# Kernel optimization log

Measured on AMD Instinct MI355X. Metric: run time of the kernel, lower is better.

Reference implementation:

```python
import jax, jax.numpy as jnp
import numpy as np

N_NODES = 100000
N_EDGES = 1600000
NODE_DIM = 64
HIDDEN = 64
T = 11


def _init_linear(key, d_in, d_out, bias=True):
    kw, kb = jax.random.split(key)
    lim = 1.0 / np.sqrt(d_in)
    W = jax.random.uniform(kw, (d_in, d_out), jnp.float32, -lim, lim)
    if bias:
        b = jax.random.uniform(kb, (d_out,), jnp.float32, -lim, lim)
        return W, b
    return W


def setup_inputs() -> dict:
    key = jax.random.key(0)
    ks = jax.random.split(key, 10)
    x = jax.random.normal(ks[0], (N_NODES, NODE_DIM), jnp.float32)
    edge_index = jax.random.randint(ks[1], (2, N_EDGES), 0, N_NODES, jnp.int64)
    time_span = jnp.arange(T, dtype=jnp.float32)
    # SAGEConv params: W_neigh (lin_l, with bias) applied to mean-aggregated
    # neighbors, W_root (lin_r, no bias) applied to the node itself.
    W1n, b1 = _init_linear(ks[2], NODE_DIM, HIDDEN)
    W1r = _init_linear(ks[3], NODE_DIM, HIDDEN, bias=False)
    W2n, b2 = _init_linear(ks[4], HIDDEN, HIDDEN)
    W2r = _init_linear(ks[5], HIDDEN, HIDDEN, bias=False)
    W3n, b3 = _init_linear(ks[6], HIDDEN, NODE_DIM)
    W3r = _init_linear(ks[7], HIDDEN, NODE_DIM, bias=False)
    Wd, bd = _init_linear(ks[8], NODE_DIM, 2)
    return {
        "x": x, "edge_index": edge_index, "time_span": time_span,
        "W1n": W1n, "b1": b1, "W1r": W1r,
        "W2n": W2n, "b2": b2, "W2r": W2r,
        "W3n": W3n, "b3": b3, "W3r": W3r,
        "Wd": Wd, "bd": bd,
    }


def _sage_conv(x, src, dst, deg_inv, Wn, bn, Wr):
    # gather source features, mean-aggregate onto targets (PyG SAGEConv 'mean')
    agg = jax.ops.segment_sum(x[src], dst, num_segments=N_NODES)  # [N, d]
    mean = agg * deg_inv  # zero for isolated nodes
    return mean @ Wn + bn + x @ Wr


def reference(x, edge_index, time_span, W1n, b1, W1r, W2n, b2, W2r,
              W3n, b3, W3r, Wd, bd):
    src, dst = edge_index[0], edge_index[1]
    deg = jax.ops.segment_sum(jnp.ones((N_EDGES,), jnp.float32), dst,
                              num_segments=N_NODES)
    deg_inv = jnp.where(deg > 0, 1.0 / jnp.maximum(deg, 1.0), 0.0)[:, None]

    def ode_func(h):
        h1 = jax.nn.relu(_sage_conv(h, src, dst, deg_inv, W1n, b1, W1r))
        h2 = jax.nn.relu(_sage_conv(h1, src, dst, deg_inv, W2n, b2, W2r))
        return _sage_conv(h2, src, dst, deg_inv, W3n, b3, W3r)

    dts = time_span[1:] - time_span[:-1]  # euler fixed-step per interval

    def step(h, dt):
        h_new = h + dt * ode_func(h)
        return h_new, h_new

    _, xs = jax.lax.scan(step, x, dts)
    solution = jnp.concatenate([x[None], xs], axis=0)  # [T, N, node_dim]
    trajectories = solution @ Wd + bd  # [T, N, 2]
    return trajectories, solution
```

## Files before the change

### kernel.cpp

```cpp
#include <hip/hip_runtime.h>

#define NN 100000
#define NE 1600000
#define DIM 64
#define TT 11
#define NB_SCAN 391

typedef unsigned short u16;
typedef unsigned int u32;
typedef __attribute__((ext_vector_type(8))) short bf16x8;
typedef __attribute__((ext_vector_type(4))) float f32x4;

__device__ __forceinline__ u32 pack_bf16(float a, float b) {
    u32 ua = __float_as_uint(a);
    ua += 0x7fff + ((ua >> 16) & 1);
    u32 ub = __float_as_uint(b);
    ub += 0x7fff + ((ub >> 16) & 1);
    return (ua >> 16) | (ub & 0xffff0000u);
}

__global__ void k_deg(const int* __restrict__ dst, int* __restrict__ deg) {
    int e = blockIdx.x * blockDim.x + threadIdx.x;
    if (e < NE) atomicAdd(&deg[dst[e]], 1);
}

__global__ __launch_bounds__(256) void k_bsum(const int* __restrict__ deg,
                                              int* __restrict__ bsum) {
    __shared__ int s[256];
    int t = threadIdx.x;
    int i = blockIdx.x * 256 + t;
    s[t] = (i < NN) ? deg[i] : 0;
    __syncthreads();
    for (int off = 128; off >= 1; off >>= 1) {
        if (t < off) s[t] += s[t + off];
        __syncthreads();
    }
    if (t == 0) bsum[blockIdx.x] = s[0];
}

__global__ __launch_bounds__(512) void k_scan1(const int* __restrict__ bsum,
                                               int* __restrict__ bpre) {
    __shared__ int s[512];
    int t = threadIdx.x;
    int v0 = (t < NB_SCAN) ? bsum[t] : 0;
    s[t] = v0;
    __syncthreads();
    for (int off = 1; off < 512; off <<= 1) {
        int v = (t >= off) ? s[t - off] : 0;
        __syncthreads();
        s[t] += v;
        __syncthreads();
    }
    if (t < NB_SCAN) bpre[t] = s[t] - v0;
}

__global__ __launch_bounds__(256) void k_rowptr(const int* __restrict__ deg,
        const int* __restrict__ bpre, int* __restrict__ row_ptr,
        int* __restrict__ cursor, float* __restrict__ deg_inv) {
    __shared__ int s[256];
    int t = threadIdx.x;
    int i = blockIdx.x * 256 + t;
    int d = (i < NN) ? deg[i] : 0;
    s[t] = d;
    __syncthreads();
    for (int off = 1; off < 256; off <<= 1) {
        int v = (t >= off) ? s[t - off] : 0;
        __syncthreads();
        s[t] += v;
        __syncthreads();
    }
    if (i < NN) {
        int excl = bpre[blockIdx.x] + s[t] - d;
        row_ptr[i] = excl;
        cursor[i] = excl;
        deg_inv[i] = d > 0 ? 1.0f / (float)d : 0.0f;
        if (i == NN - 1) row_ptr[NN] = excl + d;
    }
}

__global__ void k_fill(const int* __restrict__ src, const int* __restrict__ dst,
        int* __restrict__ cursor, int* __restrict__ csr_src) {
    int e = blockIdx.x * blockDim.x + threadIdx.x;
    if (e < NE) {
        int p = atomicAdd(&cursor[dst[e]], 1);
        csr_src[p] = src[e];
    }
}

__global__ __launch_bounds__(256) void k_wprep(
        const float* __restrict__ W1n, const float* __restrict__ W1r,
        const float* __restrict__ W2n, const float* __restrict__ W2r,
        const float* __restrict__ W3n, const float* __restrict__ W3r,
        u16* __restrict__ Wt) {
    const float* Ws[6] = {W1n, W1r, W2n, W2r, W3n, W3r};
    const float* W = Ws[blockIdx.x];
    u16* o = Wt + blockIdx.x * 4096;
    int t = threadIdx.x;
    int n = t >> 2, kg = (t & 3) * 16;
    u32 pk[8];
#pragma unroll
    for (int j = 0; j < 8; ++j)
        pk[j] = pack_bf16(W[(kg + 2 * j) * 64 + n], W[(kg + 2 * j + 1) * 64 + n]);
    *(uint4*)(o + n * 64 + kg)     = make_uint4(pk[0], pk[1], pk[2], pk[3]);
    *(uint4*)(o + n * 64 + kg + 8) = make_uint4(pk[4], pk[5], pk[6], pk[7]);
}

__global__ __launch_bounds__(256) void k_gather(const u16* __restrict__ hb,
        const int* __restrict__ row_ptr, const int* __restrict__ csr_src,
        const float* __restrict__ deg_inv, u16* __restrict__ Mb) {
    int wid = (int)((blockIdx.x * blockDim.x + threadIdx.x) >> 6);
    int lane = threadIdx.x & 63;
    if (wid >= NN) return;
    int sub = lane >> 3;
    int d4 = lane & 7;
    int b = row_ptr[wid], e = row_ptr[wid + 1];
    float di = deg_inv[wid];
    float a0[8] = {0, 0, 0, 0, 0, 0, 0, 0};
    float a1[8] = {0, 0, 0, 0, 0, 0, 0, 0};
    int i = b;
    for (; i + 16 <= e; i += 16) {
        int n0 = csr_src[i + sub];
        int n1 = csr_src[i + 8 + sub];
        uint4 v0 = *(const uint4*)(hb + ((size_t)n0 << 6) + d4 * 8);
        uint4 v1 = *(const uint4*)(hb + ((size_t)n1 << 6) + d4 * 8);
        const u32* w0 = (const u32*)&v0;
        const u32* w1 = (const u32*)&v1;
#pragma unroll
        for (int w = 0; w < 4; ++w) {
            a0[2 * w]     += __uint_as_float(w0[w] << 16);
            a0[2 * w + 1] += __uint_as_float(w0[w] & 0xffff0000u);
            a1[2 * w]     += __uint_as_float(w1[w] << 16);
            a1[2 * w + 1] += __uint_as_float(w1[w] & 0xffff0000u);
        }
    }
    if (i + 8 <= e) {
        int n0 = csr_src[i + sub];
        uint4 v0 = *(const uint4*)(hb + ((size_t)n0 << 6) + d4 * 8);
        const u32* w0 = (const u32*)&v0;
#pragma unroll
        for (int w = 0; w < 4; ++w) {
            a0[2 * w]     += __uint_as_float(w0[w] << 16);
            a0[2 * w + 1] += __uint_as_float(w0[w] & 0xffff0000u);
        }
        i += 8;
    }
    if (sub < e - i) {
        int n1 = csr_src[i + sub];
        uint4 v1 = *(const uint4*)(hb + ((size_t)n1 << 6) + d4 * 8);
        const u32* w1 = (const u32*)&v1;
#pragma unroll
        for (int w = 0; w < 4; ++w) {
            a1[2 * w]     += __uint_as_float(w1[w] << 16);
            a1[2 * w + 1] += __uint_as_float(w1[w] & 0xffff0000u);
        }
    }
    float s[8];
#pragma unroll
    for (int k = 0; k < 8; ++k) {
        float v = a0[k] + a1[k];
        v += __shfl_xor(v, 32);
        v += __shfl_xor(v, 16);
        v += __shfl_xor(v, 8);
        s[k] = v * di;
    }
    if (lane < 8) {
        uint4 p;
        p.x = pack_bf16(s[0], s[1]);
        p.y = pack_bf16(s[2], s[3]);
        p.z = pack_bf16(s[4], s[5]);
        p.w = pack_bf16(s[6], s[7]);
        *(uint4*)(Mb + ((size_t)wid << 6) + d4 * 8) = p;
    }
}

template <int MODE>
__global__ __launch_bounds__(256) void k_transform(
        const u16* __restrict__ Mb, const u16* __restrict__ Hb,
        const u16* __restrict__ Wtn, const float* __restrict__ bias,
        const u16* __restrict__ Wtr, const float* __restrict__ prev,
        const float* __restrict__ ts, int tstep, float* __restrict__ out,
        u16* __restrict__ out_b,
        const float* __restrict__ Wd, const float* __restrict__ bd,
        float* __restrict__ traj) {
    __shared__ float Ls[4][32 * 68];
    __shared__ float WdS[128];
    int tid = threadIdx.x;
    if (MODE == 1 && tid < 128) WdS[tid] = Wd[tid];
    int wv = tid >> 6, lane = tid & 63;
    int r16 = lane & 15, kq = lane >> 4;
    int nodeW = blockIdx.x * 128 + wv * 32;
    size_t rowA[2];
#pragma unroll
    for (int rt = 0; rt < 2; ++rt) {
        int n = nodeW + rt * 16 + r16;
        rowA[rt] = (size_t)(n < NN ? n : NN - 1) << 6;
    }
    f32x4 acc[2][4];
#pragma unroll
    for (int ct = 0; ct < 4; ++ct) {
        float bc = bias[ct * 16 + r16];
#pragma unroll
        for (int rt = 0; rt < 2; ++rt)
            acc[rt][ct] = (f32x4){bc, bc, bc, bc};
    }
    {
        bf16x8 a[2][2], b[4][2];
#pragma unroll
        for (int rt = 0; rt < 2; ++rt)
#pragma unroll
            for (int kh = 0; kh < 2; ++kh)
                a[rt][kh] = *(const bf16x8*)(Mb + rowA[rt] + kh * 32 + kq * 8);
#pragma unroll
        for (int ct = 0; ct < 4; ++ct)
#pragma unroll
            for (int kh = 0; kh < 2; ++kh)
                b[ct][kh] = *(const bf16x8*)(Wtn + (ct * 16 + r16) * 64 + kh * 32 + kq * 8);
#pragma unroll
        for (int rt = 0; rt < 2; ++rt)
#pragma unroll
            for (int ct = 0; ct < 4; ++ct)
#pragma unroll
                for (int kh = 0; kh < 2; ++kh)
                    acc[rt][ct] = __builtin_amdgcn_mfma_f32_16x16x32_bf16(
                        a[rt][kh], b[ct][kh], acc[rt][ct], 0, 0, 0);
    }
    {
        bf16x8 a[2][2], b[4][2];
#pragma unroll
        for (int rt = 0; rt < 2; ++rt)
#pragma unroll
            for (int kh = 0; kh < 2; ++kh)
                a[rt][kh] = *(const bf16x8*)(Hb + rowA[rt] + kh * 32 + kq * 8);
#pragma unroll
        for (int ct = 0; ct < 4; ++ct)
#pragma unroll
            for (int kh = 0; kh < 2; ++kh)
                b[ct][kh] = *(const bf16x8*)(Wtr + (ct * 16 + r16) * 64 + kh * 32 + kq * 8);
#pragma unroll
        for (int rt = 0; rt < 2; ++rt)
#pragma unroll
            for (int ct = 0; ct < 4; ++ct)
#pragma unroll
                for (int kh = 0; kh < 2; ++kh)
                    acc[rt][ct] = __builtin_amdgcn_mfma_f32_16x16x32_bf16(
                        a[rt][kh], b[ct][kh], acc[rt][ct], 0, 0, 0);
    }
    float* L = Ls[wv];
#pragma unroll
    for (int rt = 0; rt < 2; ++rt)
#pragma unroll
        for (int ct = 0; ct < 4; ++ct)
#pragma unroll
            for (int j = 0; j < 4; ++j)
                L[(rt * 16 + kq * 4 + j) * 68 + ct * 16 + r16] = acc[rt][ct][j];
    __syncthreads();
    int nl = tid >> 1, hf = tid & 1;
    int gnode = blockIdx.x * 128 + nl;
    const float* Lrow = &Ls[nl >> 5][(nl & 31) * 68 + hf * 32];
    float dt = 0.f;
    if (MODE == 1) dt = ts[tstep + 1] - ts[tstep];
    float v[32];
    float p0 = 0.f, p1 = 0.f;
    bool ok = gnode < NN;
    size_t gofs = ((size_t)(ok ? gnode : 0) << 6) + hf * 32;
#pragma unroll
    for (int i = 0; i < 32; ++i) {
        float x = Lrow[i];
        if (MODE == 0) x = fmaxf(x, 0.f);
        v[i] = x;
    }
    if (MODE == 1) {
#pragma unroll
        for (int i4 = 0; i4 < 8; ++i4) {
            float4 pv = *(const float4*)(prev + gofs + i4 * 4);
            v[i4 * 4 + 0] = pv.x + dt * v[i4 * 4 + 0];
            v[i4 * 4 + 1] = pv.y + dt * v[i4 * 4 + 1];
            v[i4 * 4 + 2] = pv.z + dt * v[i4 * 4 + 2];
            v[i4 * 4 + 3] = pv.w + dt * v[i4 * 4 + 3];
        }
#pragma unroll
        for (int i = 0; i < 32; ++i) {
            p0 = fmaf(v[i], WdS[(hf * 32 + i) * 2 + 0], p0);
            p1 = fmaf(v[i], WdS[(hf * 32 + i) * 2 + 1], p1);
        }
    }
    if (ok) {
        if (MODE == 1) {
#pragma unroll
            for (int i4 = 0; i4 < 8; ++i4)
                *(float4*)(out + gofs + i4 * 4) =
                    make_float4(v[i4 * 4], v[i4 * 4 + 1], v[i4 * 4 + 2], v[i4 * 4 + 3]);
        }
#pragma unroll
        for (int q = 0; q < 2; ++q) {
            uint4 pb;
            pb.x = pack_bf16(v[q * 16 + 0], v[q * 16 + 1]);
            pb.y = pack_bf16(v[q * 16 + 2], v[q * 16 + 3]);
            pb.z = pack_bf16(v[q * 16 + 4], v[q * 16 + 5]);
            pb.w = pack_bf16(v[q * 16 + 6], v[q * 16 + 7]);
            uint4 pc;
            pc.x = pack_bf16(v[q * 16 + 8], v[q * 16 + 9]);
            pc.y = pack_bf16(v[q * 16 + 10], v[q * 16 + 11]);
            pc.z = pack_bf16(v[q * 16 + 12], v[q * 16 + 13]);
            pc.w = pack_bf16(v[q * 16 + 14], v[q * 16 + 15]);
            *(uint4*)(out_b + gofs + q * 16)     = pb;
            *(uint4*)(out_b + gofs + q * 16 + 8) = pc;
        }
    }
    if (MODE == 1) {
        p0 += __shfl_xor(p0, 1);
        p1 += __shfl_xor(p1, 1);
        if (ok) {
            size_t ti = ((size_t)(tstep + 1) * NN + gnode) * 2;
            if (hf == 0) traj[ti + 0] = p0 + bd[0];
            else         traj[ti + 1] = p1 + bd[1];
        }
    }
}

__global__ __launch_bounds__(256) void k_init(const float* __restrict__ x,
        const float* __restrict__ Wd, const float* __restrict__ bd,
        float* __restrict__ sol0, u16* __restrict__ xb,
        float* __restrict__ traj) {
    int n = blockIdx.x * blockDim.x + threadIdx.x;
    if (n >= NN) return;
    const float4* xr = (const float4*)(x + ((size_t)n << 6));
    float4* sr = (float4*)(sol0 + ((size_t)n << 6));
    uint4* br = (uint4*)(xb + ((size_t)n << 6));
    float p0 = bd[0], p1 = bd[1];
#pragma unroll
    for (int k8 = 0; k8 < 8; ++k8) {
        float4 v0 = xr[k8 * 2];
        float4 v1 = xr[k8 * 2 + 1];
        sr[k8 * 2] = v0;
        sr[k8 * 2 + 1] = v1;
        uint4 pb;
        pb.x = pack_bf16(v0.x, v0.y);
        pb.y = pack_bf16(v0.z, v0.w);
        pb.z = pack_bf16(v1.x, v1.y);
        pb.w = pack_bf16(v1.z, v1.w);
        br[k8] = pb;
        int k = k8 * 8;
        p0 = fmaf(v0.x, Wd[(k + 0) * 2], p0); p1 = fmaf(v0.x, Wd[(k + 0) * 2 + 1], p1);
        p0 = fmaf(v0.y, Wd[(k + 1) * 2], p0); p1 = fmaf(v0.y, Wd[(k + 1) * 2 + 1], p1);
        p0 = fmaf(v0.z, Wd[(k + 2) * 2], p0); p1 = fmaf(v0.z, Wd[(k + 2) * 2 + 1], p1);
        p0 = fmaf(v0.w, Wd[(k + 3) * 2], p0); p1 = fmaf(v0.w, Wd[(k + 3) * 2 + 1], p1);
        p0 = fmaf(v1.x, Wd[(k + 4) * 2], p0); p1 = fmaf(v1.x, Wd[(k + 4) * 2 + 1], p1);
        p0 = fmaf(v1.y, Wd[(k + 5) * 2], p0); p1 = fmaf(v1.y, Wd[(k + 5) * 2 + 1], p1);
        p0 = fmaf(v1.z, Wd[(k + 6) * 2], p0); p1 = fmaf(v1.z, Wd[(k + 6) * 2 + 1], p1);
        p0 = fmaf(v1.w, Wd[(k + 7) * 2], p0); p1 = fmaf(v1.w, Wd[(k + 7) * 2 + 1], p1);
    }
    traj[(size_t)n * 2 + 0] = p0;
    traj[(size_t)n * 2 + 1] = p1;
}

extern "C" void kernel_launch(void* const* d_in, const int* in_sizes, int n_in,
                              void* d_out, int out_size, void* d_ws, size_t ws_size,
                              hipStream_t stream) {
    const float* x = (const float*)d_in[0];
    const int* ei = (const int*)d_in[1];
    const float* ts = (const float*)d_in[2];
    const float* W1n = (const float*)d_in[3];
    const float* b1 = (const float*)d_in[4];
    const float* W1r = (const float*)d_in[5];
    const float* W2n = (const float*)d_in[6];
    const float* b2 = (const float*)d_in[7];
    const float* W2r = (const float*)d_in[8];
    const float* W3n = (const float*)d_in[9];
    const float* b3 = (const float*)d_in[10];
    const float* W3r = (const float*)d_in[11];
    const float* Wd = (const float*)d_in[12];
    const float* bd = (const float*)d_in[13];
    const int* src = ei;
    const int* dst = ei + NE;

    char* w = (char*)d_ws;
    int* deg = (int*)w;          w += (size_t)NN * 4;
    int* row_ptr = (int*)w;      w += (size_t)(NN + 1) * 4;
    int* cursor = (int*)w;       w += (size_t)NN * 4;
    float* deg_inv = (float*)w;  w += (size_t)NN * 4;
    int* bsum = (int*)w;         w += (size_t)512 * 4;
    int* bpre = (int*)w;         w += (size_t)512 * 4;
    int* csr = (int*)w;          w += (size_t)NE * 4;
    u16* Wt = (u16*)w;           w += (size_t)6 * 4096 * 2;
    u16* Mb = (u16*)w;           w += (size_t)NN * DIM * 2;
    u16* hb0 = (u16*)w;          w += (size_t)NN * DIM * 2;
    u16* hb1 = (u16*)w;          w += (size_t)NN * DIM * 2;
    u16* hb2 = (u16*)w;          w += (size_t)NN * DIM * 2;

    float* traj = (float*)d_out;
    float* sol = traj + (size_t)TT * NN * 2;

    hipMemsetAsync(deg, 0, (size_t)NN * 4, stream);
    k_deg<<<(NE + 255) / 256, 256, 0, stream>>>(dst, deg);
    k_bsum<<<NB_SCAN, 256, 0, stream>>>(deg, bsum);
    k_scan1<<<1, 512, 0, stream>>>(bsum, bpre);
    k_rowptr<<<NB_SCAN, 256, 0, stream>>>(deg, bpre, row_ptr, cursor, deg_inv);
    k_fill<<<(NE + 255) / 256, 256, 0, stream>>>(src, dst, cursor, csr);
    k_wprep<<<6, 256, 0, stream>>>(W1n, W1r, W2n, W2r, W3n, W3r, Wt);
    k_init<<<NB_SCAN, 256, 0, stream>>>(x, Wd, bd, sol, hb0, traj);

    const u16* Wt1n = Wt;
    const u16* Wt1r = Wt + 4096;
    const u16* Wt2n = Wt + 2 * 4096;
    const u16* Wt2r = Wt + 3 * 4096;
    const u16* Wt3n = Wt + 4 * 4096;
    const u16* Wt3r = Wt + 5 * 4096;

    const int GB = (NN * 64 + 255) / 256;
    const int TB = (NN + 127) / 128;
    for (int t = 0; t < TT - 1; ++t) {
        float* st = sol + (size_t)t * NN * DIM;
        float* sn = st + (size_t)NN * DIM;
        k_gather<<<GB, 256, 0, stream>>>(hb0, row_ptr, csr, deg_inv, Mb);
        k_transform<0><<<TB, 256, 0, stream>>>(Mb, hb0, Wt1n, b1, Wt1r, nullptr,
                ts, t, nullptr, hb1, Wd, bd, traj);
        k_gather<<<GB, 256, 0, stream>>>(hb1, row_ptr, csr, deg_inv, Mb);
        k_transform<0><<<TB, 256, 0, stream>>>(Mb, hb1, Wt2n, b2, Wt2r, nullptr,
                ts, t, nullptr, hb2, Wd, bd, traj);
        k_gather<<<GB, 256, 0, stream>>>(hb2, row_ptr, csr, deg_inv, Mb);
        k_transform<1><<<TB, 256, 0, stream>>>(Mb, hb2, Wt3n, b3, Wt3r, st,
                ts, t, sn, hb0, Wd, bd, traj);
    }
}
```

Measured before the change: 2.287 ms.

## Assign one node per 8-lane group in gather instead of one per wavefront

The neighbor-mean gather kernel now maps 8 nodes to each 64-lane wavefront, with each 8-lane group walking its own node's edge list four neighbors at a time. Previously a whole wavefront handled one node and needed cross-lane shuffles for the reduction. This drops the shuffles and lanes that sat idle on low-degree nodes, and puts more independent loads in flight per lane. In exchange, lanes in a wavefront now diverge on differing degrees, the per-thread edge loop is serial, and the grid size relies on NN dividing exactly by 32 with no bounds check.

```diff
diff --git a/kernel.cpp b/kernel.cpp
--- a/kernel.cpp
+++ b/kernel.cpp
@@ -110,67 +110,60 @@
         const float* __restrict__ deg_inv, u16* __restrict__ Mb) {
     int wid = (int)((blockIdx.x * blockDim.x + threadIdx.x) >> 6);
     int lane = threadIdx.x & 63;
-    if (wid >= NN) return;
-    int sub = lane >> 3;
-    int d4 = lane & 7;
-    int b = row_ptr[wid], e = row_ptr[wid + 1];
-    float di = deg_inv[wid];
+    int g = lane >> 3, d4 = lane & 7;
+    int row = wid * 8 + g;
+    int b = row_ptr[row], e = row_ptr[row + 1];
+    float di = deg_inv[row];
     float a0[8] = {0, 0, 0, 0, 0, 0, 0, 0};
     float a1[8] = {0, 0, 0, 0, 0, 0, 0, 0};
+    float a2[8] = {0, 0, 0, 0, 0, 0, 0, 0};
+    float a3[8] = {0, 0, 0, 0, 0, 0, 0, 0};
     int i = b;
-    for (; i + 16 <= e; i += 16) {
-        int n0 = csr_src[i + sub];
-        int n1 = csr_src[i + 8 + sub];
-        uint4 v0 = *(const uint4*)(hb + ((size_t)n0 << 6) + d4 * 8);
-        uint4 v1 = *(const uint4*)(hb + ((size_t)n1 << 6) + d4 * 8);
+    for (; i + 4 <= e; i += 4) {
+        int n0 = csr_src[i];
+        int n1 = csr_src[i + 1];
+        int n2 = csr_src[i + 2];
+        int n3 = csr_src[i + 3];
+        uint4 v0 = *(const uint4*)(hb + ((size_t)n0 << 6) + (d4 << 3));
+        uint4 v1 = *(const uint4*)(hb + ((size_t)n1 << 6) + (d4 << 3));
+        uint4 v2 = *(const uint4*)(hb + ((size_t)n2 << 6) + (d4 << 3));
+        uint4 v3 = *(const uint4*)(hb + ((size_t)n3 << 6) + (d4 << 3));
         const u32* w0 = (const u32*)&v0;
         const u32* w1 = (const u32*)&v1;
+        const u32* w2 = (const u32*)&v2;
+        const u32* w3 = (const u32*)&v3;
 #pragma unroll
         for (int w = 0; w < 4; ++w) {
             a0[2 * w]     += __uint_as_float(w0[w] << 16);
             a0[2 * w + 1] += __uint_as_float(w0[w] & 0xffff0000u);
             a1[2 * w]     += __uint_as_float(w1[w] << 16);
             a1[2 * w + 1] += __uint_as_float(w1[w] & 0xffff0000u);
-        }
-    }
-    if (i + 8 <= e) {
-        int n0 = csr_src[i + sub];
-        uint4 v0 = *(const uint4*)(hb + ((size_t)n0 << 6) + d4 * 8);
+            a2[2 * w]     += __uint_as_float(w2[w] << 16);
+            a2[2 * w + 1] += __uint_as_float(w2[w] & 0xffff0000u);
+            a3[2 * w]     += __uint_as_float(w3[w] << 16);
+            a3[2 * w + 1] += __uint_as_float(w3[w] & 0xffff0000u);
+        }
+    }
+    for (; i < e; ++i) {
+        int n0 = csr_src[i];
+        uint4 v0 = *(const uint4*)(hb + ((size_t)n0 << 6) + (d4 << 3));
         const u32* w0 = (const u32*)&v0;
 #pragma unroll
         for (int w = 0; w < 4; ++w) {
             a0[2 * w]     += __uint_as_float(w0[w] << 16);
             a0[2 * w + 1] += __uint_as_float(w0[w] & 0xffff0000u);
         }
-        i += 8;
-    }
-    if (sub < e - i) {
-        int n1 = csr_src[i + sub];
-        uint4 v1 = *(const uint4*)(hb + ((size_t)n1 << 6) + d4 * 8);
-        const u32* w1 = (const u32*)&v1;
-#pragma unroll
-        for (int w = 0; w < 4; ++w) {
-            a1[2 * w]     += __uint_as_float(w1[w] << 16);
-            a1[2 * w + 1] += __uint_as_float(w1[w] & 0xffff0000u);
-        }
-    }
-    float s[8];
-#pragma unroll
-    for (int k = 0; k < 8; ++k) {
-        float v = a0[k] + a1[k];
-        v += __shfl_xor(v, 32);
-        v += __shfl_xor(v, 16);
-        v += __shfl_xor(v, 8);
-        s[k] = v * di;
-    }
-    if (lane < 8) {
-        uint4 p;
-        p.x = pack_bf16(s[0], s[1]);
-        p.y = pack_bf16(s[2], s[3]);
-        p.z = pack_bf16(s[4], s[5]);
-        p.w = pack_bf16(s[6], s[7]);
-        *(uint4*)(Mb + ((size_t)wid << 6) + d4 * 8) = p;
-    }
+    }
+    uint4 p;
+    p.x = pack_bf16(((a0[0] + a1[0]) + (a2[0] + a3[0])) * di,
+                    ((a0[1] + a1[1]) + (a2[1] + a3[1])) * di);
+    p.y = pack_bf16(((a0[2] + a1[2]) + (a2[2] + a3[2])) * di,
+                    ((a0[3] + a1[3]) + (a2[3] + a3[3])) * di);
+    p.z = pack_bf16(((a0[4] + a1[4]) + (a2[4] + a3[4])) * di,
+                    ((a0[5] + a1[5]) + (a2[5] + a3[5])) * di);
+    p.w = pack_bf16(((a0[6] + a1[6]) + (a2[6] + a3[6])) * di,
+                    ((a0[7] + a1[7]) + (a2[7] + a3[7])) * di);
+    *(uint4*)(Mb + ((size_t)row << 6) + (d4 << 3)) = p;
 }
 
 template <int MODE>
@@ -407,7 +400,7 @@
     const u16* Wt3n = Wt + 4 * 4096;
     const u16* Wt3r = Wt + 5 * 4096;
 
-    const int GB = (NN * 64 + 255) / 256;
+    const int GB = NN / 8 / 4;
     const int TB = (NN + 127) / 128;
     for (int t = 0; t < TT - 1; ++t) {
         float* st = sol + (size_t)t * NN * DIM;
```

Result: no change. 2.331 ms (+2.0%).
